# Kernel tuning notes

Measured on AMD Instinct MI355X. Metric: run time of the kernel, lower is better.

The kernel has to match this reference:

```python
import jax, jax.numpy as jnp
from jax import lax
import numpy as np

N, I, O = 64, 8, 8
B = 512
S_EX, S_PHI, S_RHO = 10, 60, 60  # S_phi must equal S_rho (alpha loops feed S_rho-sized h into the GRUs)
N_ACTIONS, N_ROLES = 5, 7


def _gru(x, h, Wih, Whh, bih, bhh):
    # torch.nn.GRUCell math
    gi = x @ Wih.T + bih
    gh = h @ Whh.T + bhh
    ir, iz, inn = jnp.split(gi, 3, axis=-1)
    hr, hz, hn = jnp.split(gh, 3, axis=-1)
    r = jax.nn.sigmoid(ir + hr)
    zg = jax.nn.sigmoid(iz + hz)
    n = jnp.tanh(inn + r * hn)
    return (1.0 - zg) * n + zg * h


def setup_inputs() -> dict:
    key = jax.random.key(0)
    ks = jax.random.split(key, 24)
    f32 = jnp.float32
    z = jax.random.normal(ks[0], (B, N, S_EX), f32)
    dz = jax.random.normal(ks[1], (B, N, S_EX), f32)
    has = (jax.random.uniform(ks[2], (B, N)) < 0.9).astype(f32)
    adj = (jnp.triu(jax.random.uniform(ks[3], (N, N)), 1) > 0.7).astype(jnp.int32)

    def lin(k, o, i):
        return (jax.random.normal(k, (o, i), f32) * np.float32(1.0 / np.sqrt(i)))

    d = dict(z=z, dz=dz, has=has, adj=adj)
    d['Wih_f'] = lin(ks[4], 3 * S_PHI, S_RHO)
    d['Whh_f'] = lin(ks[5], 3 * S_PHI, S_PHI)
    d['bih_f'] = jax.random.normal(ks[6], (3 * S_PHI,), f32) * 0.02
    d['bhh_f'] = jax.random.normal(ks[7], (3 * S_PHI,), f32) * 0.02
    d['Wih_b'] = lin(ks[8], 3 * S_PHI, S_RHO)
    d['Whh_b'] = lin(ks[9], 3 * S_PHI, S_PHI)
    d['bih_b'] = jax.random.normal(ks[10], (3 * S_PHI,), f32) * 0.02
    d['bhh_b'] = jax.random.normal(ks[11], (3 * S_PHI,), f32) * 0.02
    d['Wf'] = lin(ks[12], S_RHO, S_PHI + 2 * S_EX)
    d['bf'] = jax.random.normal(ks[13], (S_RHO,), f32) * 0.02
    d['Wb'] = lin(ks[14], S_RHO, S_PHI + 2 * S_EX)
    d['bb'] = jax.random.normal(ks[15], (S_RHO,), f32) * 0.02
    d['Wa'] = lin(ks[16], N_ACTIONS, 2 * S_PHI)
    d['ba'] = jax.random.normal(ks[17], (N_ACTIONS,), f32) * 0.02
    d['Wc'] = lin(ks[18], 1, 2 * S_PHI)
    d['bc'] = jax.random.normal(ks[19], (1,), f32) * 0.02
    d['Wu'] = lin(ks[20], N_ROLES, 2 * S_RHO)
    d['bu'] = jax.random.normal(ks[21], (N_ROLES,), f32) * 0.02
    return d


def reference(z, dz, has, adj,
              Wih_f, Whh_f, bih_f, bhh_f,
              Wih_b, Whh_b, bih_b, bhh_b,
              Wf, bf, Wb, bb, Wa, ba, Wc, bc, Wu, bu):
    Bn, Nn = has.shape
    dt = z.dtype
    adjf = adj.astype(dt)

    # ---- forward sweep over nodes in ascending order ----
    def fwd_outer(rho, i):
        def inner(h, j):
            hn = _gru(rho[j], h, Wih_f, Whh_f, bih_f, bhh_f)
            blend = adjf[j, i] * has[:, j][:, None]  # edge exists AND source node present
            return h + blend * (hn - h), None
        h, _ = lax.scan(inner, jnp.zeros((Bn, S_PHI), dt), jnp.arange(Nn))
        rho_i = jnp.tanh(jnp.concatenate([h, z[:, i], dz[:, i]], 1) @ Wf.T + bf)
        return rho.at[i].set(rho_i), None

    rho_f, _ = lax.scan(fwd_outer, jnp.zeros((Nn, Bn, S_RHO), dt), jnp.arange(Nn))

    # ---- backward sweep over nodes in descending order ----
    def bwd_outer(rho, i):
        def inner(h, j):
            hn = _gru(rho[j], h, Wih_b, Whh_b, bih_b, bhh_b)
            blend = adjf[i, j] * has[:, j][:, None]  # out-edges of i, visited descending
            return h + blend * (hn - h), None
        h, _ = lax.scan(inner, jnp.zeros((Bn, S_PHI), dt), jnp.arange(Nn - 1, -1, -1))
        rho_i = jnp.concatenate([h, z[:, i], dz[:, i]], 1) @ Wb.T + bb
        return rho.at[i].set(rho_i), None

    rho_b, _ = lax.scan(bwd_outer, jnp.zeros((Nn, Bn, S_RHO), dt), jnp.arange(Nn - 1, -1, -1))

    # ---- aggregate outputs (last O nodes) and inputs (first I nodes) ----
    h = jnp.zeros((Bn, S_RHO), dt)
    for i in range(N - O, N):
        hn = _gru(rho_f[i], h, Wih_f, Whh_f, bih_f, bhh_f)
        h = h + has[:, i][:, None] * (hn - h)
    alpha_f = h
    h = jnp.zeros((Bn, S_RHO), dt)
    for i in reversed(range(I)):
        hn = _gru(rho_b[i], h, Wih_b, Whh_b, bih_b, bhh_b)
        h = h + has[:, i][:, None] * (hn - h)
    alpha_b = h

    ab = jnp.concatenate([alpha_f, alpha_b], 1)
    omega = ab @ Wa.T + ba          # [B, 5]
    value = ab @ Wc.T + bc          # [B, 1]

    feats = jnp.concatenate([rho_f, rho_b], -1)           # [N, B, 2*S_rho]
    psi = jnp.einsum('nbs,rs->brn', feats, Wu) + bu[None, :, None]  # [B, 7, N]
    m = has[:, None, :]
    psi = -60.0 * (1.0 - m) + psi * m  # interpolate(-60, psi, has)

    instr_prob = jax.nn.softmax(omega, axis=1)
    role_prob = jax.nn.softmax(psi, axis=2)
    return instr_prob, role_prob, value
```

## Files before the change

kernel.cpp:

```cpp
#include <hip/hip_runtime.h>
#include <hip/hip_bf16.h>

#define NN 64
#define BATCH 512
#define SP 60
#define SG 180
#define SEX 10
#define CATD 80
#define NA 5
#define NR 7
#define OO 8
#define II 8

typedef unsigned long long u64;
typedef unsigned short u16;
typedef unsigned int u32;
typedef unsigned char u8;

#define OFF_Z     0
#define OFF_DZ    327680
#define OFF_HAS   655360
#define OFF_WIHF  688128
#define OFF_WHHF  698928
#define OFF_BIHF  709728
#define OFF_BHHF  709908
#define OFF_WIHB  710088
#define OFF_WHHB  720888
#define OFF_BIHB  731688
#define OFF_BHHB  731868
#define OFF_WF    732048
#define OFF_BF    736848
#define OFF_WB    736908
#define OFF_BB    741708
#define OFF_WA    741768
#define OFF_BA    742368
#define OFF_WC    742373
#define OFF_BC    742493
#define OFF_WU    742494
#define OFF_BU    743334
#define CONV_TOTAL 743341
#define OFF_FLAG  743342
#define OFF_RHOF  743344
#define OFF_RHOB  (OFF_RHOF + 1966080)
#define OFF_ALF   (OFF_RHOB + 1966080)
#define OFF_ALB   (OFF_ALF + 30720)
#define OUT_TOTAL 232448

typedef _Float16 f16;
typedef _Float16 half2_t __attribute__((ext_vector_type(2)));
typedef _Float16 f16x8 __attribute__((ext_vector_type(8)));
typedef float f32x4 __attribute__((ext_vector_type(4)));

__device__ __forceinline__ float us2f(u16 v){
  return __uint_as_float(((u32)v) << 16);
}
__device__ __forceinline__ u16 f2bf(float f){
  __hip_bfloat16 h = __float2bfloat16(f);
  return *reinterpret_cast<u16*>(&h);
}
__device__ __forceinline__ float rcp_(float x){ return __builtin_amdgcn_rcpf(x); }
__device__ __forceinline__ float sigm(float x){
  return rcp_(1.f + __expf(-x));
}
__device__ __forceinline__ float tanh_(float x){
  float e = __expf(2.f*fabsf(x));
  float t = 1.f - 2.f*rcp_(e + 1.f);
  return copysignf(t, x);
}
__device__ __forceinline__ u32 pack2(float a, float b){
  half2_t h; h[0] = (f16)a; h[1] = (f16)b;
  return __builtin_bit_cast(u32, h);
}
__device__ __forceinline__ float fdot2_(u32 a, u32 b, float c){
  return __builtin_amdgcn_fdot2(__builtin_bit_cast(half2_t, a),
                                __builtin_bit_cast(half2_t, b), c, false);
}
__device__ __forceinline__ f16x8 bc16(uint4 v){ return __builtin_bit_cast(f16x8, v); }
__device__ __forceinline__ f32x4 mfma16(f16x8 a, f16x8 b, f32x4 c){
  return __builtin_amdgcn_mfma_f32_16x16x32_f16(a, b, c, 0, 0, 0);
}

__device__ __forceinline__ int detect_bf16(const u32* w){
  int f = 0;
  for (int i=0;i<256;i++) f |= (w[i] == 0x3F803F80u) ? 1 : 0;
  return f;
}

__global__ __launch_bounds__(256) void conv_in(
  const void* z, const void* dz, const void* has,
  const void* WihF, const void* WhhF, const void* bihF, const void* bhhF,
  const void* WihB, const void* WhhB, const void* bihB, const void* bhhB,
  const void* Wf_, const void* bf_, const void* Wb_, const void* bb_,
  const void* Wa, const void* ba, const void* Wc, const void* bc,
  const void* Wu, const void* bu, float* ws)
{
  const int isbf = detect_bf16((const u32*)has);
  if (blockIdx.x == 0 && threadIdx.x == 0) ws[OFF_FLAG] = (float)isbf;
  int idx = blockIdx.x*256 + threadIdx.x;
  if (idx >= CONV_TOTAL) return;
  const void* src; int loc;
  if      (idx < OFF_DZ  ){ src=z;    loc=idx-OFF_Z;    }
  else if (idx < OFF_HAS ){ src=dz;   loc=idx-OFF_DZ;   }
  else if (idx < OFF_WIHF){ src=has;  loc=idx-OFF_HAS;  }
  else if (idx < OFF_WHHF){ src=WihF; loc=idx-OFF_WIHF; }
  else if (idx < OFF_BIHF){ src=WhhF; loc=idx-OFF_WHHF; }
  else if (idx < OFF_BHHF){ src=bihF; loc=idx-OFF_BIHF; }
  else if (idx < OFF_WIHB){ src=bhhF; loc=idx-OFF_BHHF; }
  else if (idx < OFF_WHHB){ src=WihB; loc=idx-OFF_WIHB; }
  else if (idx < OFF_BIHB){ src=WhhB; loc=idx-OFF_WHHB; }
  else if (idx < OFF_BHHB){ src=bihB; loc=idx-OFF_BIHB; }
  else if (idx < OFF_WF  ){ src=bhhB; loc=idx-OFF_BHHB; }
  else if (idx < OFF_BF  ){ src=Wf_;  loc=idx-OFF_WF;   }
  else if (idx < OFF_WB  ){ src=bf_;  loc=idx-OFF_BF;   }
  else if (idx < OFF_BB  ){ src=Wb_;  loc=idx-OFF_WB;   }
  else if (idx < OFF_WA  ){ src=bb_;  loc=idx-OFF_BB;   }
  else if (idx < OFF_BA  ){ src=Wa;   loc=idx-OFF_WA;   }
  else if (idx < OFF_WC  ){ src=ba;   loc=idx-OFF_BA;   }
  else if (idx < OFF_BC  ){ src=Wc;   loc=idx-OFF_WC;   }
  else if (idx < OFF_WU  ){ src=bc;   loc=idx-OFF_BC;   }
  else if (idx < OFF_BU  ){ src=Wu;   loc=idx-OFF_WU;   }
  else                    { src=bu;   loc=idx-OFF_BU;   }
  float v = isbf ? us2f(((const u16*)src)[loc]) : ((const float*)src)[loc];
  ws[idx] = v;
}

__global__ __launch_bounds__(256, 4) void dir_kernel(const int* __restrict__ adj,
                                                     float* __restrict__ ws)
{
  const int tid = threadIdx.x;
  const int w   = tid >> 6;
  const int u   = tid & 63;
  const int ml  = u & 15;
  const int q   = u >> 4;
  const int bid = blockIdx.x;
  const int bwd = bid >> 9;
  const int b   = bid & 511;

  const float* Wih  = ws + (bwd ? OFF_WIHB : OFF_WIHF);
  const float* Whh  = ws + (bwd ? OFF_WHHB : OFF_WHHF);
  const float* bih  = ws + (bwd ? OFF_BIHB : OFF_BIHF);
  const float* bhh  = ws + (bwd ? OFF_BHHB : OFF_BHHF);
  const float* Wcat = ws + (bwd ? OFF_WB   : OFF_WF);
  const float* bcat = ws + (bwd ? OFF_BB   : OFF_BF);
  const float* zc   = ws + OFF_Z;
  const float* dzc  = ws + OFF_DZ;
  const float* hasc = ws + OFF_HAS;
  float* rho   = ws + (bwd ? OFF_RHOB : OFF_RHOF);
  float* alpha = ws + (bwd ? OFF_ALB  : OFF_ALF);

  __shared__ uint4 sH4[65][9];
  __shared__ uint4 sRhoPad[8];
  __shared__ uint4 sRhoHist[8][8];
  __shared__ float sZdc[NN][SP];
  __shared__ float sPart[4][64];
  __shared__ u32 sZp[NN][5];
  __shared__ u32 sDZp[NN][5];
  __shared__ float sHas[NN];
  __shared__ u64 sRowM[NN];
  __shared__ u8 sConsL[NN][64];
  __shared__ int sConsCnt[NN];

  #define ROWB(I) ((char*)&sH4[(I)][0])
  const u32 BIASW = 0x3C000000u;

  {
    if (tid < 64){
      u64 rowm = 0;
      for (int j=0;j<64;j++) rowm |= ((u64)(adj[tid*64+j]!=0))<<j;
      sRowM[tid] = rowm;
      sHas[tid] = hasc[b*NN + tid];
    }
    for (int idx=tid; idx<65*9; idx+=256){
      uint4 v = {0,0,0,0};
      if (idx % 9 == 7) v.w = BIASW;
      ((uint4*)sH4)[idx] = v;
    }
    if (tid < 8){ uint4 v={0,0,0,0}; if (tid==7) v.w = BIASW; sRhoPad[tid]=v; }
    if (tid < 64){ uint4 v={0,0,0,0}; if ((tid&7)==7) v.w = BIASW; ((uint4*)sRhoHist)[tid]=v; }
    for (int idx=tid; idx<NN*5; idx+=256){
      int n2=idx/5, p2=idx%5;
      sZp [n2][p2] = pack2(zc [(size_t)b*NN*SEX + n2*SEX + 2*p2],
                           zc [(size_t)b*NN*SEX + n2*SEX + 2*p2+1]);
      sDZp[n2][p2] = pack2(dzc[(size_t)b*NN*SEX + n2*SEX + 2*p2],
                           dzc[(size_t)b*NN*SEX + n2*SEX + 2*p2+1]);
    }
  }
  __syncthreads();
  if (tid < 64){
    u64 cm = 0;
    if (bwd) for (int i2=0;i2<64;i2++) cm |= ((sRowM[i2]>>tid)&1ULL)<<i2;
    u64 m = bwd ? cm : sRowM[tid];
    int c = 0;
    while (m){ int i2 = (int)__builtin_ctzll(m); m &= m-1; sConsL[tid][c++] = (u8)i2; }
    sConsCnt[tid] = c;
  }
  {
    const int uu = tid & 63;
    const int tw = tid >> 6;
    if (uu < SP){
      u32 wz[10];
      #pragma unroll
      for (int p=0;p<10;p++)
        wz[p] = pack2(Wcat[uu*CATD + 60 + 2*p], Wcat[uu*CATD + 60 + 2*p + 1]);
      const float bb0 = bcat[uu];
      for (int t2=tw; t2<NN; t2+=4){
        float c = bb0;
        #pragma unroll
        for (int p=0;p<5;p++){
          c = fdot2_(wz[p],   sZp [t2][p], c);
          c = fdot2_(wz[5+p], sDZp[t2][p], c);
        }
        sZdc[t2][uu] = c;
      }
    }
  }

  f16x8 Ar[4], Az[4], Anh[2], Ani[2];
  {
    const int R = 16*w + ml;
    const bool rok = (R < SP);
    #pragma unroll
    for (int kt=0; kt<4; kt++){
      f16x8 vr, vz;
      #pragma unroll
      for (int j=0;j<8;j++){
        const int K = 32*kt + 8*q + j;
        float wr=0.f, wz2=0.f;
        if (rok){
          if (K < SP){ wr = Whh[R*SP+K]; wz2 = Whh[(60+R)*SP+K]; }
          else if (K >= 64 && K < 64+SP){ wr = Wih[R*SP+(K-64)]; wz2 = Wih[(60+R)*SP+(K-64)]; }
          else if (K == 127){ wr = bhh[R]+bih[R]; wz2 = bhh[60+R]+bih[60+R]; }
        }
        vr[j]=(f16)wr; vz[j]=(f16)wz2;
      }
      Ar[kt]=vr; Az[kt]=vz;
    }
    #pragma unroll
    for (int kt=0; kt<2; kt++){
      f16x8 vn, vi;
      #pragma unroll
      for (int j=0;j<8;j++){
        const int K = 32*kt + 8*q + j;
        float wn=0.f, wi=0.f;
        if (rok){
          if (K < SP){ wn = Whh[(120+R)*SP+K]; wi = Wih[(120+R)*SP+K]; }
          else if (K == 63){ wn = bhh[120+R]; wi = bih[120+R]; }
        }
        vn[j]=(f16)wn; vi[j]=(f16)wi;
      }
      Anh[kt]=vn; Ani[kt]=vi;
    }
  }

  u32 wc[8];
  #pragma unroll
  for (int k=0;k<8;k++){
    const int kk = 8*w + k;
    wc[k] = (kk < 30) ? pack2(Wcat[u*CATD + 2*kk], Wcat[u*CATD + 2*kk + 1]) : 0u;
  }
  __syncthreads();

  auto gates = [&](f32x4 Dr, f32x4 Dz, f32x4 Dn, f32x4 Gn,
                   int ci, bool wr, float bl){
    char* rp = ROWB(ci) + 32*w + 8*q;
    uint2 h2 = *(uint2*)rp;
    half2_t ha = __builtin_bit_cast(half2_t, h2.x);
    half2_t hb = __builtin_bit_cast(half2_t, h2.y);
    float hold[4] = { (float)ha[0], (float)ha[1], (float)hb[0], (float)hb[1] };
    float hw[4];
    #pragma unroll
    for (int reg=0;reg<4;reg++){
      float r_ = sigm(Dr[reg]);
      float zg = sigm(Dz[reg]);
      float nv = tanh_(Gn[reg] + r_*Dn[reg]);
      float hn_ = (1.f - zg)*nv + zg*hold[reg];
      hw[reg] = (bl != 0.f) ? hn_ : hold[reg];
    }
    if (wr && !(w==3 && q==3)){
      uint2 o; o.x = pack2(hw[0],hw[1]); o.y = pack2(hw[2],hw[3]);
      *(uint2*)rp = o;
    }
  };

  auto fullpass = [&](f16x8 Bh0, f16x8 Bh1, f16x8 Br0, f16x8 Br1,
                      f32x4 Gn, int ci, bool wr, float bl){
    f32x4 Dr={0,0,0,0}, Dz={0,0,0,0}, Dn={0,0,0,0};
    Dr = mfma16(Ar[0], Bh0, Dr); Dr = mfma16(Ar[1], Bh1, Dr);
    Dr = mfma16(Ar[2], Br0, Dr); Dr = mfma16(Ar[3], Br1, Dr);
    Dz = mfma16(Az[0], Bh0, Dz); Dz = mfma16(Az[1], Bh1, Dz);
    Dz = mfma16(Az[2], Br0, Dz); Dz = mfma16(Az[3], Br1, Dz);
    Dn = mfma16(Anh[0], Bh0, Dn); Dn = mfma16(Anh[1], Bh1, Dn);
    gates(Dr, Dz, Dn, Gn, ci, wr, bl);
  };

  int t = bwd ? 63 : 0;
  const int dt = bwd ? -1 : 1;
  for (int s=0; s<64; s++, t+=dt){
    const float blendT = sHas[t];
    const int cnt = sConsCnt[t];
    const bool act = (blendT != 0.f) && (cnt > 0);
    const bool g1  = act && (cnt > 16);

    f32x4 Dr={0,0,0,0}, Dz={0,0,0,0}, Dn={0,0,0,0};
    f32x4 Dr2={0,0,0,0}, Dz2={0,0,0,0}, Dn2={0,0,0,0};
    int ci0 = 64, ci1 = 64;
    if (act){
      ci0 = (ml < cnt) ? (int)sConsL[t][ml] : 64;
      const f16x8 Bh0 = bc16(sH4[ci0][q]);
      const f16x8 Bh1 = bc16(sH4[ci0][4+q]);
      Dr = mfma16(Ar[0], Bh0, Dr); Dr = mfma16(Ar[1], Bh1, Dr);
      Dz = mfma16(Az[0], Bh0, Dz); Dz = mfma16(Az[1], Bh1, Dz);
      Dn = mfma16(Anh[0], Bh0, Dn); Dn = mfma16(Anh[1], Bh1, Dn);
      if (g1){
        ci1 = (16 + ml < cnt) ? (int)sConsL[t][16 + ml] : 64;
        const f16x8 Ch0 = bc16(sH4[ci1][q]);
        const f16x8 Ch1 = bc16(sH4[ci1][4+q]);
        Dr2 = mfma16(Ar[0], Ch0, Dr2); Dr2 = mfma16(Ar[1], Ch1, Dr2);
        Dz2 = mfma16(Az[0], Ch0, Dz2); Dz2 = mfma16(Az[1], Ch1, Dz2);
        Dn2 = mfma16(Anh[0], Ch0, Dn2); Dn2 = mfma16(Anh[1], Ch1, Dn2);
      }
    }

    {
      const uint4* hr = &sH4[t][0];
      uint4 ha = hr[2*w];
      uint4 hb = hr[2*w+1];
      float cA = 0.f;
      float cB = (w == 3) ? ((u < SP) ? sZdc[t][u] : 0.f) : 0.f;
      cA = fdot2_(wc[0], ha.x, cA); cB = fdot2_(wc[1], ha.y, cB);
      cA = fdot2_(wc[2], ha.z, cA); cB = fdot2_(wc[3], ha.w, cB);
      cA = fdot2_(wc[4], hb.x, cA); cB = fdot2_(wc[5], hb.y, cB);
      if (w < 3){ cA = fdot2_(wc[6], hb.z, cA); cB = fdot2_(wc[7], hb.w, cB); }
      sPart[w][u] = cA + cB;
    }
    __syncthreads();

    if (w == 0){
      float acc = (sPart[0][u] + sPart[1][u]) + (sPart[2][u] + sPart[3][u]);
      float rv = bwd ? acc : tanh_(acc);
      if (u < SP){
        rho[((size_t)t*BATCH + b)*SP + u] = rv;
        *(f16*)((char*)&sRhoPad[0] + 2*u) = (f16)rv;
      }
      const int slot = bwd ? t : (t - (NN-OO));
      if (slot >= 0 && slot < 8 && u < SP)
        *(f16*)((char*)&sRhoHist[slot][0] + 2*u) = (f16)rv;
    }
    __syncthreads();

    if (act){
      const f16x8 Br0 = bc16(sRhoPad[q]);
      const f16x8 Br1 = bc16(sRhoPad[4+q]);
      f32x4 Gn={0,0,0,0};
      Gn = mfma16(Ani[0], Br0, Gn);
      Gn = mfma16(Ani[1], Br1, Gn);

      Dr = mfma16(Ar[2], Br0, Dr); Dr = mfma16(Ar[3], Br1, Dr);
      Dz = mfma16(Az[2], Br0, Dz); Dz = mfma16(Az[3], Br1, Dz);
      gates(Dr, Dz, Dn, Gn, ci0, ml < cnt, 1.0f);

      if (g1){
        Dr2 = mfma16(Ar[2], Br0, Dr2); Dr2 = mfma16(Ar[3], Br1, Dr2);
        Dz2 = mfma16(Az[2], Br0, Dz2); Dz2 = mfma16(Az[3], Br1, Dz2);
        gates(Dr2, Dz2, Dn2, Gn, ci1, 16 + ml < cnt, 1.0f);
      }

      for (int p=2; 16*p < cnt; p++){
        const int idxp = 16*p + ml;
        const int ci = (idxp < cnt) ? (int)sConsL[t][idxp] : 64;
        const f16x8 Bh0 = bc16(sH4[ci][q]);
        const f16x8 Bh1 = bc16(sH4[ci][4+q]);
        fullpass(Bh0, Bh1, Br0, Br1, Gn, ci, idxp < cnt, 1.0f);
      }
    }
    __syncthreads();
  }

  for (int s2=0; s2<8; s2++){
    const int i = bwd ? (7 - s2) : (NN - OO + s2);
    const int slot = bwd ? i : (i - (NN-OO));
    const f16x8 Th0 = bc16(sH4[64][q]);
    const f16x8 Th1 = bc16(sH4[64][4+q]);
    const f16x8 Tr0 = bc16(sRhoHist[slot][q]);
    const f16x8 Tr1 = bc16(sRhoHist[slot][4+q]);
    f32x4 Gt={0,0,0,0};
    Gt = mfma16(Ani[0], Tr0, Gt);
    Gt = mfma16(Ani[1], Tr1, Gt);
    __syncthreads();
    fullpass(Th0, Th1, Tr0, Tr1, Gt, 64, ml==0, sHas[i]);
    __syncthreads();
  }
  if (tid < SP) alpha[(size_t)b*SP + tid] = (float)*(const f16*)(ROWB(64) + 2*tid);
  #undef ROWB
}

__global__ __launch_bounds__(256, 1) void head_kernel(float* __restrict__ ws,
                                                      void* __restrict__ outp)
{
  const int b = blockIdx.x;
  const int tid = threadIdx.x;
  const int isbf = (ws[OFF_FLAG] != 0.f);
  const float* hasc   = ws + OFF_HAS;
  const float* WaC    = ws + OFF_WA;
  const float* baC    = ws + OFF_BA;
  const float* WcC    = ws + OFF_WC;
  const float* bcC    = ws + OFF_BC;
  const float* WuC    = ws + OFF_WU;
  const float* buC    = ws + OFF_BU;
  const float* rhoF   = ws + OFF_RHOF;
  const float* rhoB   = ws + OFF_RHOB;
  const float* alphaF = ws + OFF_ALF;
  const float* alphaB = ws + OFF_ALB;

  __shared__ float sF[NN][121];
  __shared__ float sAB[120];
  __shared__ float sWu[NR*120];
  __shared__ float sHasR[NN];
  __shared__ float sPsi[NR][NN];
  __shared__ float sRed[NR][2];
  __shared__ float sOm[NA];

  auto wout = [&](int idx, float v){
    if (isbf) ((u16*)outp)[idx] = f2bf(v);
    else      ((float*)outp)[idx] = v;
  };

  for (int idx=tid; idx<NN*SP; idx+=256){
    int n = idx/SP, s = idx%SP;
    sF[n][s]    = rhoF[((size_t)n*BATCH + b)*SP + s];
    sF[n][60+s] = rhoB[((size_t)n*BATCH + b)*SP + s];
  }
  for (int idx=tid; idx<120; idx+=256)
    sAB[idx] = (idx<60) ? alphaF[(size_t)b*SP + idx] : alphaB[(size_t)b*SP + idx-60];
  for (int idx=tid; idx<NR*120; idx+=256) sWu[idx] = WuC[idx];
  for (int idx=tid; idx<NN; idx+=256) sHasR[idx] = hasc[b*NN + idx];
  __syncthreads();

  for (int idx=tid; idx<NR*NN; idx+=256){
    int r = idx/NN, n = idx%NN;
    float acc = buC[r];
    for (int s=0;s<120;s++) acc += sF[n][s]*sWu[r*120+s];
    sPsi[r][n] = (sHasR[n] != 0.f) ? acc : -60.f;
  }
  if (tid >= 64 && tid < 64+NA){
    int a = tid - 64;
    float acc = baC[a];
    for (int s=0;s<120;s++) acc += sAB[s]*WaC[a*120+s];
    sOm[a] = acc;
  }
  if (tid == 70){
    float acc = bcC[0];
    for (int s=0;s<120;s++) acc += sAB[s]*WcC[s];
    wout(2560 + BATCH*NR*NN + b, acc);
  }
  __syncthreads();

  if (tid < NR){
    float m = -1e30f;
    for (int n=0;n<NN;n++) m = fmaxf(m, sPsi[tid][n]);
    float ssum = 0.f;
    for (int n=0;n<NN;n++) ssum += __expf(sPsi[tid][n]-m);
    sRed[tid][0] = m; sRed[tid][1] = 1.f/ssum;
  }
  if (tid == 8){
    float m = -1e30f;
    for (int a=0;a<NA;a++) m = fmaxf(m, sOm[a]);
    float e[NA]; float ssum = 0.f;
    for (int a=0;a<NA;a++){ e[a] = __expf(sOm[a]-m); ssum += e[a]; }
    for (int a=0;a<NA;a++) wout(b*NA + a, e[a]/ssum);
  }
  __syncthreads();

  for (int idx=tid; idx<NR*NN; idx+=256){
    int r = idx/NN, n = idx%NN;
    float v = __expf(sPsi[r][n]-sRed[r][0]) * sRed[r][1];
    wout(2560 + (size_t)b*NR*NN + idx, v);
  }
}

extern "C" void kernel_launch(void* const* d_in, const int* in_sizes, int n_in,
                              void* d_out, int out_size, void* d_ws, size_t ws_size,
                              hipStream_t stream)
{
  const int* adj = (const int*)d_in[3];
  float* ws = (float*)d_ws;

  conv_in<<<(CONV_TOTAL+255)/256, 256, 0, stream>>>(
      d_in[0], d_in[1], d_in[2],
      d_in[4], d_in[5], d_in[6], d_in[7],
      d_in[8], d_in[9], d_in[10], d_in[11],
      d_in[12], d_in[13], d_in[14], d_in[15],
      d_in[16], d_in[17], d_in[18], d_in[19],
      d_in[20], d_in[21], ws);

  dir_kernel<<<1024, 256, 0, stream>>>(adj, ws);

  head_kernel<<<512, 256, 0, stream>>>(ws, d_out);
}
```

Measured before the change: 281.7 us.

## Compute rho projection with MFMA and drop cross-wave partial-sum reduction

Replaces the per-step rho projection (fdot2 partial sums across four waves, a shared sPart buffer, an extra barrier and a wave-0 reduction) with a two-MFMA matrix product per wave. Each wave now writes its own rho rows directly, which removes one __syncthreads per timestep from the serial 64-step recurrence. The rho contribution to the r and z gates is computed once and reused for both consumer groups. The consumer-h MFMAs are moved after the barrier, so the gate work now happens in a single phase after rho is ready; this reduces overlap with the rho computation but shortens the critical path. The Wcat weights are converted to f16 for the MFMA, which may shift precision slightly.

```diff
diff --git a/kernel.cpp b/kernel.cpp
--- a/kernel.cpp
+++ b/kernel.cpp
@@ -151,8 +151,7 @@
   __shared__ uint4 sH4[65][9];
   __shared__ uint4 sRhoPad[8];
   __shared__ uint4 sRhoHist[8][8];
-  __shared__ float sZdc[NN][SP];
-  __shared__ float sPart[4][64];
+  __shared__ float sZdc[NN][64];
   __shared__ u32 sZp[NN][5];
   __shared__ u32 sDZp[NN][5];
   __shared__ float sHas[NN];
@@ -215,7 +214,7 @@
     }
   }
 
-  f16x8 Ar[4], Az[4], Anh[2], Ani[2];
+  f16x8 Ar[4], Az[4], Anh[2], Ani[2], Ac[2];
   {
     const int R = 16*w + ml;
     const bool rok = (R < SP);
@@ -237,26 +236,19 @@
     }
     #pragma unroll
     for (int kt=0; kt<2; kt++){
-      f16x8 vn, vi;
+      f16x8 vn, vi, vc;
       #pragma unroll
       for (int j=0;j<8;j++){
         const int K = 32*kt + 8*q + j;
-        float wn=0.f, wi=0.f;
+        float wn=0.f, wi=0.f, wcv=0.f;
         if (rok){
-          if (K < SP){ wn = Whh[(120+R)*SP+K]; wi = Wih[(120+R)*SP+K]; }
+          if (K < SP){ wn = Whh[(120+R)*SP+K]; wi = Wih[(120+R)*SP+K]; wcv = Wcat[R*CATD+K]; }
           else if (K == 63){ wn = bhh[120+R]; wi = bih[120+R]; }
         }
-        vn[j]=(f16)wn; vi[j]=(f16)wi;
-      }
-      Anh[kt]=vn; Ani[kt]=vi;
-    }
-  }
-
-  u32 wc[8];
-  #pragma unroll
-  for (int k=0;k<8;k++){
-    const int kk = 8*w + k;
-    wc[k] = (kk < 30) ? pack2(Wcat[u*CATD + 2*kk], Wcat[u*CATD + 2*kk + 1]) : 0u;
+        vn[j]=(f16)wn; vi[j]=(f16)wi; vc[j]=(f16)wcv;
+      }
+      Anh[kt]=vn; Ani[kt]=vi; Ac[kt]=vc;
+    }
   }
   __syncthreads();
 
@@ -301,50 +293,39 @@
     const bool act = (blendT != 0.f) && (cnt > 0);
     const bool g1  = act && (cnt > 16);
 
-    f32x4 Dr={0,0,0,0}, Dz={0,0,0,0}, Dn={0,0,0,0};
-    f32x4 Dr2={0,0,0,0}, Dz2={0,0,0,0}, Dn2={0,0,0,0};
     int ci0 = 64, ci1 = 64;
+    f16x8 Bh0g0={}, Bh1g0={}, Bh0g1={}, Bh1g1={};
     if (act){
       ci0 = (ml < cnt) ? (int)sConsL[t][ml] : 64;
-      const f16x8 Bh0 = bc16(sH4[ci0][q]);
-      const f16x8 Bh1 = bc16(sH4[ci0][4+q]);
-      Dr = mfma16(Ar[0], Bh0, Dr); Dr = mfma16(Ar[1], Bh1, Dr);
-      Dz = mfma16(Az[0], Bh0, Dz); Dz = mfma16(Az[1], Bh1, Dz);
-      Dn = mfma16(Anh[0], Bh0, Dn); Dn = mfma16(Anh[1], Bh1, Dn);
+      Bh0g0 = bc16(sH4[ci0][q]);
+      Bh1g0 = bc16(sH4[ci0][4+q]);
       if (g1){
         ci1 = (16 + ml < cnt) ? (int)sConsL[t][16 + ml] : 64;
-        const f16x8 Ch0 = bc16(sH4[ci1][q]);
-        const f16x8 Ch1 = bc16(sH4[ci1][4+q]);
-        Dr2 = mfma16(Ar[0], Ch0, Dr2); Dr2 = mfma16(Ar[1], Ch1, Dr2);
-        Dz2 = mfma16(Az[0], Ch0, Dz2); Dz2 = mfma16(Az[1], Ch1, Dz2);
-        Dn2 = mfma16(Anh[0], Ch0, Dn2); Dn2 = mfma16(Anh[1], Ch1, Dn2);
+        Bh0g1 = bc16(sH4[ci1][q]);
+        Bh1g1 = bc16(sH4[ci1][4+q]);
       }
     }
 
     {
-      const uint4* hr = &sH4[t][0];
-      uint4 ha = hr[2*w];
-      uint4 hb = hr[2*w+1];
-      float cA = 0.f;
-      float cB = (w == 3) ? ((u < SP) ? sZdc[t][u] : 0.f) : 0.f;
-      cA = fdot2_(wc[0], ha.x, cA); cB = fdot2_(wc[1], ha.y, cB);
-      cA = fdot2_(wc[2], ha.z, cA); cB = fdot2_(wc[3], ha.w, cB);
-      cA = fdot2_(wc[4], hb.x, cA); cB = fdot2_(wc[5], hb.y, cB);
-      if (w < 3){ cA = fdot2_(wc[6], hb.z, cA); cB = fdot2_(wc[7], hb.w, cB); }
-      sPart[w][u] = cA + cB;
-    }
-    __syncthreads();
-
-    if (w == 0){
-      float acc = (sPart[0][u] + sPart[1][u]) + (sPart[2][u] + sPart[3][u]);
-      float rv = bwd ? acc : tanh_(acc);
-      if (u < SP){
-        rho[((size_t)t*BATCH + b)*SP + u] = rv;
-        *(f16*)((char*)&sRhoPad[0] + 2*u) = (f16)rv;
-      }
-      const int slot = bwd ? t : (t - (NN-OO));
-      if (slot >= 0 && slot < 8 && u < SP)
-        *(f16*)((char*)&sRhoHist[slot][0] + 2*u) = (f16)rv;
+      const f16x8 Hb0 = bc16(sH4[t][q]);
+      const f16x8 Hb1 = bc16(sH4[t][4+q]);
+      f32x4 Rv = {0,0,0,0};
+      Rv = mfma16(Ac[0], Hb0, Rv);
+      Rv = mfma16(Ac[1], Hb1, Rv);
+      const int row = 16*w + 4*q + ml;
+      if (ml < 4 && row < SP){
+        float vv = Rv[0];
+        vv = (ml==1) ? Rv[1] : vv;
+        vv = (ml==2) ? Rv[2] : vv;
+        vv = (ml==3) ? Rv[3] : vv;
+        vv += sZdc[t][row];
+        if (!bwd) vv = tanh_(vv);
+        *(f16*)((char*)&sRhoPad[0] + 2*row) = (f16)vv;
+        const int slot = bwd ? t : (t - (NN-OO));
+        if (slot >= 0 && slot < 8)
+          *(f16*)((char*)&sRhoHist[slot][0] + 2*row) = (f16)vv;
+        rho[((size_t)t*BATCH + b)*SP + row] = vv;
+      }
     }
     __syncthreads();
 
@@ -352,19 +333,26 @@
       const f16x8 Br0 = bc16(sRhoPad[q]);
       const f16x8 Br1 = bc16(sRhoPad[4+q]);
       f32x4 Gn={0,0,0,0};
-      Gn = mfma16(Ani[0], Br0, Gn);
-      Gn = mfma16(Ani[1], Br1, Gn);
-
-      Dr = mfma16(Ar[2], Br0, Dr); Dr = mfma16(Ar[3], Br1, Dr);
-      Dz = mfma16(Az[2], Br0, Dz); Dz = mfma16(Az[3], Br1, Dz);
-      gates(Dr, Dz, Dn, Gn, ci0, ml < cnt, 1.0f);
-
+      Gn = mfma16(Ani[0], Br0, Gn); Gn = mfma16(Ani[1], Br1, Gn);
+      f32x4 Pr={0,0,0,0};
+      Pr = mfma16(Ar[2], Br0, Pr); Pr = mfma16(Ar[3], Br1, Pr);
+      f32x4 Pz={0,0,0,0};
+      Pz = mfma16(Az[2], Br0, Pz); Pz = mfma16(Az[3], Br1, Pz);
+
+      {
+        f32x4 Dr=Pr, Dz=Pz, Dn={0,0,0,0};
+        Dr = mfma16(Ar[0], Bh0g0, Dr); Dr = mfma16(Ar[1], Bh1g0, Dr);
+        Dz = mfma16(Az[0], Bh0g0, Dz); Dz = mfma16(Az[1], Bh1g0, Dz);
+        Dn = mfma16(Anh[0], Bh0g0, Dn); Dn = mfma16(Anh[1], Bh1g0, Dn);
+        gates(Dr, Dz, Dn, Gn, ci0, ml < cnt, 1.0f);
+      }
       if (g1){
-        Dr2 = mfma16(Ar[2], Br0, Dr2); Dr2 = mfma16(Ar[3], Br1, Dr2);
-        Dz2 = mfma16(Az[2], Br0, Dz2); Dz2 = mfma16(Az[3], Br1, Dz2);
-        gates(Dr2, Dz2, Dn2, Gn, ci1, 16 + ml < cnt, 1.0f);
-      }
-
+        f32x4 Dr=Pr, Dz=Pz, Dn={0,0,0,0};
+        Dr = mfma16(Ar[0], Bh0g1, Dr); Dr = mfma16(Ar[1], Bh1g1, Dr);
+        Dz = mfma16(Az[0], Bh0g1, Dz); Dz = mfma16(Az[1], Bh1g1, Dz);
+        Dn = mfma16(Anh[0], Bh0g1, Dn); Dn = mfma16(Anh[1], Bh1g1, Dn);
+        gates(Dr, Dz, Dn, Gn, ci1, 16 + ml < cnt, 1.0f);
+      }
       for (int p=2; 16*p < cnt; p++){
         const int idxp = 16*p + ml;
         const int ci = (idxp < cnt) ? (int)sConsL[t][idxp] : 64;
```

Result: faster. 272.9 us (-3.1%).
